# Performance work log

Hardware: AMD Instinct MI355X
Metric: run time of the kernel (lower is better)

## Reference

```python
import jax, jax.numpy as jnp
import numpy as np

TOP_K = 2
CAPACITY_FACTOR = 1.0


def setup_inputs() -> dict:
    key = jax.random.key(0)
    ks = jax.random.split(key, 4)
    sl, bs, hs, ffn, E = 2048, 8, 1024, 4096, 8
    x = jax.random.normal(ks[0], (sl, bs, hs), dtype=jnp.float32)
    w_router = jax.random.normal(ks[1], (hs, E), dtype=jnp.float32) * 0.02
    w1 = jax.random.normal(ks[2], (E, hs, ffn), dtype=jnp.float32) * 0.02
    w2 = jax.random.normal(ks[3], (E, ffn, hs), dtype=jnp.float32) * 0.02
    bias = jnp.zeros((1, 1, hs), dtype=jnp.float32)
    return {"x": x, "w_router": w_router, "w1": w1, "w2": w2, "bias": bias}


def reference(x, w_router, w1, w2, bias):
    sl, bs, hs = x.shape
    E = w_router.shape[1]
    xf = x.reshape(-1, hs)                     # [T, hs]
    T = xf.shape[0]
    capacity = int(CAPACITY_FACTOR * TOP_K * T / E)  # static expert capacity

    # LearnedRouter: softmax over expert logits, then top-k
    scores = jax.nn.softmax(xf @ w_router, axis=-1)          # [T, E]
    expert_weights, top_experts = jax.lax.top_k(scores, TOP_K)

    flat_e = top_experts.reshape(-1)           # [N] N = T*top_k
    flat_w = expert_weights.reshape(-1)
    N = flat_e.shape[0]

    # ops.sort (stable radix sort) + ops.histogram + inclusive_cumsum
    order = jnp.argsort(flat_e, stable=True)   # indices
    bin_ids = flat_e[order]
    tpe = jnp.zeros((E,), jnp.int32).at[flat_e].add(1)       # tokens_per_expert
    starts = jnp.cumsum(tpe) - tpe             # exclusive bin starts
    offsets = jnp.arange(N) - starts[bin_ids]  # position within expert bin

    # binned_gather: first `capacity` tokens per expert, rest dropped
    valid = offsets < capacity
    slot = jnp.where(valid, bin_ids * capacity + offsets, E * capacity)
    src = order // TOP_K                       # source token row for each slot
    xb = jnp.zeros((E * capacity + 1, hs), x.dtype).at[slot].set(xf[src])
    xb = xb[:-1].reshape(E, capacity, hs)

    # grouped MLP (megablocks mlp.MLP): gelu between two grouped GEMMs
    h = jax.nn.gelu(jnp.einsum('ech,ehf->ecf', xb, w1))
    y = jnp.einsum('ecf,efh->ech', h, w2).reshape(E * capacity, hs)

    # binned_scatter: weighted combine back to token order (dropped -> 0)
    yv = jnp.where(valid[:, None], y[jnp.minimum(slot, E * capacity - 1)], 0.0)
    out = jnp.zeros((T, hs), x.dtype).at[src].add(flat_w[order][:, None] * yv)
    return out.reshape(sl, bs, hs) + bias
```

## Files before the change

### kernel.cpp

```cpp
#include <hip/hip_runtime.h>
#include <stdint.h>
#include <math.h>

typedef unsigned short u16;
typedef __attribute__((ext_vector_type(8))) short bf16x8;
typedef __attribute__((ext_vector_type(4))) float f32x4;

#define HS   1024
#define NEXP 8
#define FFN  4096

__device__ __forceinline__ u16 f2b(float f) {
  uint32_t u = __builtin_bit_cast(uint32_t, f);
  u = (u + 0x7fffu + ((u >> 16) & 1u)) >> 16;
  return (u16)u;
}
__device__ __forceinline__ float gelu_tanh(float x) {
  float z = 0.7978845608028654f * (x + 0.044715f * x * x * x);
  float e = __expf(2.0f * z);
  return 0.5f * x * (1.0f + (1.0f - 2.0f / (e + 1.0f)));
}
__device__ __forceinline__ void gload_lds16(const void* g, void* l) {
  __builtin_amdgcn_global_load_lds(
      (__attribute__((address_space(1))) void*)(void*)g,
      (__attribute__((address_space(3))) void*)l, 16, 0, 0);
}

__global__ __launch_bounds__(256) void convert_bf16(const float* __restrict__ in,
                                                    u16* __restrict__ out) {
  const int i = (blockIdx.x * 256 + threadIdx.x) * 4;
  float4 v = *(const float4*)(in + i);
  ushort4 o;
  o.x = f2b(v.x); o.y = f2b(v.y); o.z = f2b(v.z); o.w = f2b(v.w);
  *(ushort4*)(out + i) = o;
}

__global__ __launch_bounds__(256) void transpose_convert(const float* __restrict__ in,
                                                         u16* __restrict__ out,
                                                         int K, int N) {
  __shared__ u16 tile[32][33];
  const int z = blockIdx.z;
  const int k0 = blockIdx.y * 32, n0 = blockIdx.x * 32;
  const int tx = threadIdx.x & 31, ty = threadIdx.x >> 5;
  const float* src = in + (size_t)z * K * N;
  u16* dst = out + (size_t)z * N * K;
#pragma unroll
  for (int i = 0; i < 4; ++i)
    tile[ty + i * 8][tx] = f2b(src[(size_t)(k0 + ty + i * 8) * N + n0 + tx]);
  __syncthreads();
#pragma unroll
  for (int i = 0; i < 4; ++i)
    dst[(size_t)(n0 + ty + i * 8) * K + k0 + tx] = tile[tx][ty + i * 8];
}

__global__ __launch_bounds__(256) void router_kernel(const float* __restrict__ x,
                                                     const float* __restrict__ wr,
                                                     int T, int* __restrict__ experts,
                                                     float* __restrict__ weights) {
  const int wave = threadIdx.x >> 6, lane = threadIdx.x & 63;
  const int t = blockIdx.x * 4 + wave;
  if (t >= T) return;
  const float* xr = x + (size_t)t * HS;
  double acc[8] = {0, 0, 0, 0, 0, 0, 0, 0};
#pragma unroll
  for (int i = 0; i < HS / 64; ++i) {
    const int hrow = i * 64 + lane;
    double xv = (double)xr[hrow];
    float4 w0 = *(const float4*)(wr + hrow * 8);
    float4 w1 = *(const float4*)(wr + hrow * 8 + 4);
    acc[0] += xv * (double)w0.x; acc[1] += xv * (double)w0.y;
    acc[2] += xv * (double)w0.z; acc[3] += xv * (double)w0.w;
    acc[4] += xv * (double)w1.x; acc[5] += xv * (double)w1.y;
    acc[6] += xv * (double)w1.z; acc[7] += xv * (double)w1.w;
  }
#pragma unroll
  for (int e = 0; e < 8; ++e) {
    double v = acc[e];
#pragma unroll
    for (int off = 32; off > 0; off >>= 1) v += __shfl_xor(v, off, 64);
    acc[e] = v;
  }
  if (lane == 0) {
    double m = acc[0];
#pragma unroll
    for (int e = 1; e < 8; ++e) m = acc[e] > m ? acc[e] : m;
    double s[8], sum = 0.0;
#pragma unroll
    for (int e = 0; e < 8; ++e) { s[e] = exp(acc[e] - m); sum += s[e]; }
    double inv = 1.0 / sum;
    int e1 = 0; double l1 = acc[0];
#pragma unroll
    for (int e = 1; e < 8; ++e) if (acc[e] > l1) { l1 = acc[e]; e1 = e; }
    int e2 = -1; double l2 = -1e300;
#pragma unroll
    for (int e = 0; e < 8; ++e) if (e != e1 && acc[e] > l2) { l2 = acc[e]; e2 = e; }
    experts[2 * t] = e1;  experts[2 * t + 1] = e2;
    weights[2 * t] = (float)(s[e1] * inv);
    weights[2 * t + 1] = (float)(s[e2] * inv);
  }
}

__global__ __launch_bounds__(256) void hist_kernel(const int* __restrict__ experts,
                                                   int* __restrict__ hist,
                                                   unsigned char* __restrict__ lrank) {
  const int n = blockIdx.x * 256 + threadIdx.x;
  const int lane = threadIdx.x & 63;
  const int wid = n >> 6;
  const int e = experts[n];
  int rank = 0;
#pragma unroll
  for (int ev = 0; ev < 8; ++ev) {
    unsigned long long m = __ballot(e == ev);
    if (lane == ev) hist[wid * 8 + ev] = __popcll(m);
    if (e == ev) rank = __popcll(m & ((1ull << lane) - 1ull));
  }
  lrank[n] = (unsigned char)rank;
}

__global__ __launch_bounds__(512) void scan_kernel(const int* __restrict__ hist,
                                                   int* __restrict__ chunkBase) {
  __shared__ int s[512];
  const int tid = threadIdx.x;
  for (int e = 0; e < 8; ++e) {
    int v = hist[tid * 8 + e];
    s[tid] = v;
    __syncthreads();
    for (int off = 1; off < 512; off <<= 1) {
      int add = (tid >= off) ? s[tid - off] : 0;
      __syncthreads();
      s[tid] += add;
      __syncthreads();
    }
    chunkBase[tid * 8 + e] = s[tid] - v;
    __syncthreads();
  }
}

__global__ __launch_bounds__(256) void slot_init(int* __restrict__ rowtok,
                                                 float* __restrict__ roww) {
  const int i = blockIdx.x * 256 + threadIdx.x;
  rowtok[i] = -1;
  roww[i] = 0.0f;
}

__global__ __launch_bounds__(256) void gather_kernel(const float* __restrict__ x,
                                                     const int* __restrict__ experts,
                                                     const unsigned char* __restrict__ lrank,
                                                     const int* __restrict__ chunkBase,
                                                     const float* __restrict__ weights,
                                                     int capacity, int* __restrict__ rowtok,
                                                     float* __restrict__ roww,
                                                     u16* __restrict__ xb) {
  const int wave = threadIdx.x >> 6, lane = threadIdx.x & 63;
  const int n = blockIdx.x * 4 + wave;
  const int e = experts[n];
  const int off = chunkBase[(n >> 6) * 8 + e] + (int)lrank[n];
  if (off >= capacity) return;
  const int slot = e * capacity + off;
  if (lane == 0) { rowtok[slot] = n >> 1; roww[slot] = weights[n]; }
  if (xb == nullptr) return;
  const float* src = x + (size_t)(n >> 1) * HS;
  u16* dst = xb + (size_t)slot * HS;
#pragma unroll
  for (int i = 0; i < 4; ++i) {
    float4 v = *(const float4*)(src + i * 256 + lane * 4);
    ushort4 o;
    o.x = f2b(v.x); o.y = f2b(v.y); o.z = f2b(v.z); o.w = f2b(v.w);
    *(ushort4*)(dst + i * 256 + lane * 4) = o;
  }
}

__global__ __launch_bounds__(256) void bias_init(const float* __restrict__ bias,
                                                 float* __restrict__ out) {
  const int c = threadIdx.x * 4;
  *(float4*)(out + (size_t)blockIdx.x * HS + c) = *(const float4*)(bias + c);
}

#define VMCNT(n) asm volatile("s_waitcnt vmcnt(" #n ")" ::: "memory")
#define BAR() do { asm volatile("" ::: "memory"); \
                   __builtin_amdgcn_s_barrier();  \
                   asm volatile("" ::: "memory"); } while (0)

template <bool GELU, bool GATHER_A, bool SCATTER>
__global__ __launch_bounds__(512, 2) void gemm_moe(const u16* __restrict__ A,
                                                   const u16* __restrict__ Bt,
                                                   u16* __restrict__ Cout,
                                                   float* __restrict__ out,
                                                   const int* __restrict__ rowtok,
                                                   const float* __restrict__ roww,
                                                   int rtStride, int M, int Nn, int K) {
  int bn, bm, z;
  {
    const int gx = gridDim.x, gy = gridDim.y, gz = gridDim.z;
    const int nwg = gx * gy * gz;
    const int flat = (blockIdx.z * gy + blockIdx.y) * gx + blockIdx.x;
    const int q = nwg >> 3, r = nwg & 7;
    const int xcd = flat & 7, idx = flat >> 3;
    const int base = (xcd < r) ? xcd * (q + 1) : r * (q + 1) + (xcd - r) * q;
    int nid = base + idx;
    const int perz = gx * gy;
    z = nid / perz;
    int rem = nid - z * perz;
    const int GN = (gx >= 4) ? 4 : gx;
    const int grpsz = GN * gy;
    const int grp = rem / grpsz, ir = rem - grp * grpsz;
    const int bnl = ir % GN;
    bm = ir / GN;
    bn = grp * GN + bnl;
  }

  if (!GATHER_A) A += (size_t)z * M * K;
  Bt += (size_t)z * Nn * K;
  rowtok += (size_t)z * rtStride;
  roww += (size_t)z * rtStride;
  const u16* Bb = Bt + (size_t)bn * 256 * K;

  __shared__ u16 lds[65536];
  char* ldsA = (char*)lds;
  char* ldsB = ldsA + 65536;

  const int tid = threadIdx.x;
  const int lane = tid & 63;
  const int lrow = lane & 15, quad = lane >> 4;
  const int wid = tid >> 6, wm = wid >> 2, wn = wid & 3;

  const int swz = (lane & 7) << 4;
  const int kq0 = (quad * 16) ^ swz;
  const int kq1 = (64 + quad * 16) ^ swz;
  const int aBase = (wm * 128 + lrow) * 128;
  const int bBase = (wn * 64 + lrow) * 128;

  const u16 *gA[4], *gB[4];
#pragma unroll
  for (int s = 0; s < 4; ++s) {
    const int srow = s * 64 + (tid >> 3);
    const int scol = ((tid & 7) * 8) ^ ((srow & 7) << 3);
    if (GATHER_A) {
      int t = rowtok[bm * 256 + srow]; if (t < 0) t = 0;
      gA[s] = A + (size_t)t * K + scol;
    } else {
      gA[s] = A + (size_t)(bm * 256 + srow) * K + scol;
    }
    gB[s] = Bb + (size_t)srow * K + scol;
  }
  const int ldst0 = tid * 16;

#define STAGE_A(buf, half, kt) do { \
    gload_lds16(gA[(half)*2]   + (size_t)(kt) * 64, ldsA + (buf)*32768 + (half)*16384 +        ldst0); \
    gload_lds16(gA[(half)*2+1] + (size_t)(kt) * 64, ldsA + (buf)*32768 + (half)*16384 + 8192 + ldst0); \
  } while (0)
#define STAGE_B(buf, half, kt) do { \
    gload_lds16(gB[(half)*2]   + (size_t)(kt) * 64, ldsB + (buf)*32768 + (half)*16384 +        ldst0); \
    gload_lds16(gB[(half)*2+1] + (size_t)(kt) * 64, ldsB + (buf)*32768 + (half)*16384 + 8192 + ldst0); \
  } while (0)

  f32x4 acc[8][4] = {};
  bf16x8 a[8][2];

#define LOAD_A(ABUF) \
  _Pragma("unroll") \
  for (int m = 0; m < 8; ++m) { \
    a[m][0] = *(const bf16x8*)((ABUF) + aBase + m * 2048 + kq0); \
    a[m][1] = *(const bf16x8*)((ABUF) + aBase + m * 2048 + kq1); \
  }

#define PHASE(BBUF, NF, STAGE_STMT, END_STMT) do { \
    bf16x8 pb0 = *(const bf16x8*)((BBUF) + bBase + (NF) * 2048 + kq0); \
    bf16x8 pb1 = *(const bf16x8*)((BBUF) + bBase + (NF) * 2048 + kq1); \
    STAGE_STMT; \
    BAR(); \
    __builtin_amdgcn_s_setprio(1); \
    _Pragma("unroll") \
    for (int m = 0; m < 8; ++m) { \
      acc[m][NF] = __builtin_amdgcn_mfma_f32_16x16x32_bf16(a[m][0], pb0, acc[m][NF], 0, 0, 0); \
      acc[m][NF] = __builtin_amdgcn_mfma_f32_16x16x32_bf16(a[m][1], pb1, acc[m][NF], 0, 0, 0); \
    } \
    __builtin_amdgcn_s_setprio(0); \
    END_STMT; \
  } while (0)

  STAGE_A(0, 0, 0); STAGE_A(0, 1, 0);
  STAGE_B(0, 0, 0); STAGE_B(0, 1, 0);
  STAGE_A(1, 0, 1); STAGE_A(1, 1, 1);
  VMCNT(4);
  BAR();

  const int nIter = K >> 7;
  for (int I = 0; I < nIter; ++I) {
    const int T1 = 2 * I + 1;
    const bool hn = (I + 1 < nIter);
    LOAD_A(ldsA);
    PHASE(ldsB, 0, STAGE_B(1, 0, T1), ((void)0));
    PHASE(ldsB, 1, STAGE_B(1, 1, T1), ((void)0));
    PHASE(ldsB, 2, do { if (hn) STAGE_A(0, 0, T1 + 1); } while (0), ((void)0));
    PHASE(ldsB, 3, do { if (hn) STAGE_A(0, 1, T1 + 1); } while (0),
          do { if (hn) { VMCNT(4); } else { VMCNT(0); } BAR(); } while (0));
    LOAD_A(ldsA + 32768);
    PHASE(ldsB + 32768, 0, do { if (hn) STAGE_B(0, 0, T1 + 1); } while (0), ((void)0));
    PHASE(ldsB + 32768, 1, do { if (hn) STAGE_B(0, 1, T1 + 1); } while (0), ((void)0));
    PHASE(ldsB + 32768, 2, do { if (hn) STAGE_A(1, 0, T1 + 2); } while (0), ((void)0));
    PHASE(ldsB + 32768, 3, do { if (hn) STAGE_A(1, 1, T1 + 2); } while (0),
          do { if (hn) { VMCNT(4); } BAR(); } while (0));
  }

  const int rbase = bm * 256 + wm * 128 + quad * 4;
  const int cbase = bn * 256 + wn * 64 + lrow;
  if (!SCATTER) {
    u16* Cb = Cout + (size_t)z * M * Nn;
#pragma unroll
    for (int m = 0; m < 8; ++m)
#pragma unroll
      for (int nf = 0; nf < 4; ++nf)
#pragma unroll
        for (int r = 0; r < 4; ++r) {
          float v = acc[m][nf][r];
          if (GELU) v = gelu_tanh(v);
          Cb[(size_t)(rbase + m * 16 + r) * Nn + cbase + nf * 16] = f2b(v);
        }
  } else {
#pragma unroll
    for (int m = 0; m < 8; ++m)
#pragma unroll
      for (int r = 0; r < 4; ++r) {
        const int row = rbase + m * 16 + r;
        const int tok = rowtok[row];
        if (tok >= 0) {
          const float w = roww[row];
          float* op = out + (size_t)tok * HS + cbase;
#pragma unroll
          for (int nf = 0; nf < 4; ++nf)
            atomicAdd(op + nf * 16, w * acc[m][nf][r]);
        }
      }
  }
}

extern "C" void kernel_launch(void* const* d_in, const int* in_sizes, int n_in,
                              void* d_out, int out_size, void* d_ws, size_t ws_size,
                              hipStream_t stream) {
  const float* x    = (const float*)d_in[0];
  const float* wr   = (const float*)d_in[1];
  const float* w1   = (const float*)d_in[2];
  const float* w2   = (const float*)d_in[3];
  const float* bias = (const float*)d_in[4];
  float* out = (float*)d_out;

  const int T = in_sizes[0] / HS;
  const int N = T * 2;
  const int capacity = N / NEXP;
  const int nChunks = N / 64;

  char* ws = (char*)d_ws;
  int* experts = (int*)ws;                   ws += (size_t)N * 4;
  float* weights = (float*)ws;               ws += (size_t)N * 4;
  unsigned char* lrank = (unsigned char*)ws; ws += (size_t)N;
  int* hist = (int*)ws;                      ws += (size_t)nChunks * 8 * 4;
  int* chunkBase = (int*)ws;                 ws += (size_t)nChunks * 8 * 4;
  int* rowtok = (int*)ws;                    ws += (size_t)NEXP * capacity * 4;
  float* roww = (float*)ws;                  ws += (size_t)NEXP * capacity * 4;
  ws = (char*)(((uintptr_t)ws + 255) & ~(uintptr_t)255);
  size_t used = (size_t)(ws - (char*)d_ws);
  size_t avail = ws_size > used ? ws_size - used : 0;

  const size_t xbB  = (size_t)NEXP * capacity * HS * 2;
  const size_t perE = ((size_t)FFN * HS * 2) * 2 + (size_t)capacity * FFN * 2;

  int G = 0;
  for (int g = NEXP; g >= 1; g >>= 1)
    if (avail >= xbB + (size_t)g * perE) { G = g; break; }

  u16 *xb = nullptr, *xbf = nullptr, *w1t, *w2t, *h;
  if (G > 0) {
    xb  = (u16*)ws;  ws += xbB;
    w1t = (u16*)ws;  ws += (size_t)G * FFN * HS * 2;
    w2t = (u16*)ws;  ws += (size_t)G * HS * FFN * 2;
    h   = (u16*)ws;  ws += (size_t)G * capacity * FFN * 2;
  } else {
    G = 1;
    xbf = (u16*)ws;  ws += (size_t)T * HS * 2;
    w1t = (u16*)ws;  ws += (size_t)FFN * HS * 2;
    w2t = (u16*)ws;  ws += (size_t)HS * FFN * 2;
    h   = (u16*)ws;  ws += (size_t)capacity * FFN * 2;
    if ((size_t)(ws - (char*)d_ws) > ws_size) return;
    convert_bf16<<<T * HS / 1024, 256, 0, stream>>>(x, xbf);
  }

  router_kernel<<<T / 4, 256, 0, stream>>>(x, wr, T, experts, weights);
  hist_kernel<<<N / 256, 256, 0, stream>>>(experts, hist, lrank);
  scan_kernel<<<1, 512, 0, stream>>>(hist, chunkBase);
  slot_init<<<NEXP * capacity / 256, 256, 0, stream>>>(rowtok, roww);
  gather_kernel<<<N / 4, 256, 0, stream>>>(x, experts, lrank, chunkBase, weights,
                                           capacity, rowtok, roww, xb);
  bias_init<<<T, 256, 0, stream>>>(bias, out);

  for (int e0 = 0; e0 < NEXP; e0 += G) {
    const float* w1_g = w1 + (size_t)e0 * HS * FFN;
    const float* w2_g = w2 + (size_t)e0 * FFN * HS;
    const int* rt_g = rowtok + e0 * capacity;
    const float* rw_g = roww + e0 * capacity;
    transpose_convert<<<dim3(FFN / 32, HS / 32, G), 256, 0, stream>>>(w1_g, w1t, HS, FFN);
    transpose_convert<<<dim3(HS / 32, FFN / 32, G), 256, 0, stream>>>(w2_g, w2t, FFN, HS);
    if (xb != nullptr) {
      gemm_moe<true, false, false><<<dim3(FFN / 256, capacity / 256, G), 512, 0, stream>>>(
          xb + (size_t)e0 * capacity * HS, w1t, h, nullptr, rt_g, rw_g,
          capacity, capacity, FFN, HS);
    } else {
      gemm_moe<true, true, false><<<dim3(FFN / 256, capacity / 256, G), 512, 0, stream>>>(
          xbf, w1t, h, nullptr, rt_g, rw_g, capacity, capacity, FFN, HS);
    }
    gemm_moe<false, false, true><<<dim3(HS / 256, capacity / 256, G), 512, 0, stream>>>(
        h, w2t, nullptr, out, rt_g, rw_g, capacity, capacity, HS, FFN);
  }
}
```

Before: 1.044 ms.

## Restructure GEMM main loop into quadrant phases with explicit barriers and sched fences

The MoE grouped GEMM inner loop now splits each k-tile into four quadrant phases (half of M by half of N). Each phase reads only the needed A/B fragments from LDS, issues global-to-LDS staging, waits on lgkmcnt, and runs a block of MFMAs under sched_barrier fences, in the style of an 8-wave ping-pong schedule. The intent is to shrink register pressure from the A fragments and interleave LDS reads with MFMA work across waves more predictably. The cost is two barriers per phase instead of one, and moving the A staging into a single phase could expose more load latency.

```diff
diff --git a/kernel.cpp b/kernel.cpp
--- a/kernel.cpp
+++ b/kernel.cpp
@@ -177,9 +177,6 @@
 }
 
 #define VMCNT(n) asm volatile("s_waitcnt vmcnt(" #n ")" ::: "memory")
-#define BAR() do { asm volatile("" ::: "memory"); \
-                   __builtin_amdgcn_s_barrier();  \
-                   asm volatile("" ::: "memory"); } while (0)
 
 template <bool GELU, bool GATHER_A, bool SCATTER>
 __global__ __launch_bounds__(512, 2) void gemm_moe(const u16* __restrict__ A,
@@ -255,52 +252,77 @@
   } while (0)
 
   f32x4 acc[8][4] = {};
-  bf16x8 a[8][2];
-
-#define LOAD_A(ABUF) \
-  _Pragma("unroll") \
-  for (int m = 0; m < 8; ++m) { \
-    a[m][0] = *(const bf16x8*)((ABUF) + aBase + m * 2048 + kq0); \
-    a[m][1] = *(const bf16x8*)((ABUF) + aBase + m * 2048 + kq1); \
-  }
-
-#define PHASE(BBUF, NF, STAGE_STMT, END_STMT) do { \
-    bf16x8 pb0 = *(const bf16x8*)((BBUF) + bBase + (NF) * 2048 + kq0); \
-    bf16x8 pb1 = *(const bf16x8*)((BBUF) + bBase + (NF) * 2048 + kq1); \
+  bf16x8 aR[4][2];
+  bf16x8 bR[4][2];
+
+#define READ_A(MH, ABUF) do { \
+    _Pragma("unroll") \
+    for (int mm = 0; mm < 4; ++mm) { \
+      aR[mm][0] = *(const bf16x8*)((ABUF) + aBase + ((MH)*4+mm)*2048 + kq0); \
+      aR[mm][1] = *(const bf16x8*)((ABUF) + aBase + ((MH)*4+mm)*2048 + kq1); \
+    } } while (0)
+#define READ_B(NH, BBUF) do { \
+    _Pragma("unroll") \
+    for (int nn = 0; nn < 2; ++nn) { \
+      bR[(NH)*2+nn][0] = *(const bf16x8*)((BBUF) + bBase + ((NH)*2+nn)*2048 + kq0); \
+      bR[(NH)*2+nn][1] = *(const bf16x8*)((BBUF) + bBase + ((NH)*2+nn)*2048 + kq1); \
+    } } while (0)
+
+#define MFMA_Q(MH, NH) do { \
+    _Pragma("unroll") \
+    for (int mm = 0; mm < 4; ++mm) { \
+      _Pragma("unroll") \
+      for (int nn = 0; nn < 2; ++nn) { \
+        acc[(MH)*4+mm][(NH)*2+nn] = __builtin_amdgcn_mfma_f32_16x16x32_bf16( \
+            aR[mm][0], bR[(NH)*2+nn][0], acc[(MH)*4+mm][(NH)*2+nn], 0, 0, 0); \
+        acc[(MH)*4+mm][(NH)*2+nn] = __builtin_amdgcn_mfma_f32_16x16x32_bf16( \
+            aR[mm][1], bR[(NH)*2+nn][1], acc[(MH)*4+mm][(NH)*2+nn], 0, 0, 0); \
+      } \
+    } } while (0)
+
+#define PHASE_Q(MH, NH, READ_STMT, STAGE_STMT, TAIL_STMT) do { \
+    READ_STMT; \
     STAGE_STMT; \
-    BAR(); \
+    __builtin_amdgcn_s_barrier(); \
+    asm volatile("s_waitcnt lgkmcnt(0)" ::: "memory"); \
+    __builtin_amdgcn_sched_barrier(0); \
     __builtin_amdgcn_s_setprio(1); \
-    _Pragma("unroll") \
-    for (int m = 0; m < 8; ++m) { \
-      acc[m][NF] = __builtin_amdgcn_mfma_f32_16x16x32_bf16(a[m][0], pb0, acc[m][NF], 0, 0, 0); \
-      acc[m][NF] = __builtin_amdgcn_mfma_f32_16x16x32_bf16(a[m][1], pb1, acc[m][NF], 0, 0, 0); \
-    } \
+    MFMA_Q(MH, NH); \
     __builtin_amdgcn_s_setprio(0); \
-    END_STMT; \
+    TAIL_STMT; \
+    __builtin_amdgcn_s_barrier(); \
+    __builtin_amdgcn_sched_barrier(0); \
   } while (0)
 
   STAGE_A(0, 0, 0); STAGE_A(0, 1, 0);
   STAGE_B(0, 0, 0); STAGE_B(0, 1, 0);
   STAGE_A(1, 0, 1); STAGE_A(1, 1, 1);
   VMCNT(4);
-  BAR();
+  __builtin_amdgcn_s_barrier();
+  __builtin_amdgcn_sched_barrier(0);
 
   const int nIter = K >> 7;
   for (int I = 0; I < nIter; ++I) {
     const int T1 = 2 * I + 1;
     const bool hn = (I + 1 < nIter);
-    LOAD_A(ldsA);
-    PHASE(ldsB, 0, STAGE_B(1, 0, T1), ((void)0));
-    PHASE(ldsB, 1, STAGE_B(1, 1, T1), ((void)0));
-    PHASE(ldsB, 2, do { if (hn) STAGE_A(0, 0, T1 + 1); } while (0), ((void)0));
-    PHASE(ldsB, 3, do { if (hn) STAGE_A(0, 1, T1 + 1); } while (0),
-          do { if (hn) { VMCNT(4); } else { VMCNT(0); } BAR(); } while (0));
-    LOAD_A(ldsA + 32768);
-    PHASE(ldsB + 32768, 0, do { if (hn) STAGE_B(0, 0, T1 + 1); } while (0), ((void)0));
-    PHASE(ldsB + 32768, 1, do { if (hn) STAGE_B(0, 1, T1 + 1); } while (0), ((void)0));
-    PHASE(ldsB + 32768, 2, do { if (hn) STAGE_A(1, 0, T1 + 2); } while (0), ((void)0));
-    PHASE(ldsB + 32768, 3, do { if (hn) STAGE_A(1, 1, T1 + 2); } while (0),
-          do { if (hn) { VMCNT(4); } BAR(); } while (0));
+    PHASE_Q(0, 0, { READ_A(0, ldsA); READ_B(0, ldsB); },
+            STAGE_B(1, 0, T1), ((void)0));
+    PHASE_Q(0, 1, READ_B(1, ldsB),
+            STAGE_B(1, 1, T1), ((void)0));
+    PHASE_Q(1, 1, READ_A(1, ldsA),
+            ((void)0), ((void)0));
+    PHASE_Q(1, 0, ((void)0),
+            do { if (hn) { STAGE_A(0, 0, T1 + 1); STAGE_A(0, 1, T1 + 1); } } while (0),
+            do { if (hn) { VMCNT(4); } else { VMCNT(0); } } while (0));
+    PHASE_Q(0, 0, { READ_A(0, ldsA + 32768); READ_B(0, ldsB + 32768); },
+            do { if (hn) STAGE_B(0, 0, T1 + 1); } while (0), ((void)0));
+    PHASE_Q(0, 1, READ_B(1, ldsB + 32768),
+            do { if (hn) STAGE_B(0, 1, T1 + 1); } while (0), ((void)0));
+    PHASE_Q(1, 1, READ_A(1, ldsA + 32768),
+            ((void)0), ((void)0));
+    PHASE_Q(1, 0, ((void)0),
+            do { if (hn) { STAGE_A(1, 0, T1 + 2); STAGE_A(1, 1, T1 + 2); } } while (0),
+            do { if (hn) { VMCNT(4); } } while (0));
   }
 
   const int rbase = bm * 256 + wm * 128 + quad * 4;
```

Result: no change. 1.047 ms (+0.3%).
